# Performance work log

Measured on AMD Instinct MI355X. Metric: run time of the kernel, lower is better.

## Reference

```python
import jax, jax.numpy as jnp
import numpy as np

HID = 128  # hidden_channel
C = 256    # feat_channel

def conv1x1(x, w, b):
    # x: [N, Cin, H, W], w: [Cout, Cin], b: [Cout]
    return jnp.einsum('nchw,oc->nohw', x, w) + b[None, :, None, None]

def maxpool2(x):
    N, Ch, H, W = x.shape
    return x.reshape(N, Ch, H // 2, 2, W // 2, 2).max(axis=(3, 5))

def setup_inputs() -> dict:
    key = jax.random.key(0)
    ks = jax.random.split(key, 6)
    rois = jax.random.normal(ks[0], (128, C, 14, 14), dtype=jnp.float32)
    feature = jax.random.normal(ks[1], (2, C, 64, 64), dtype=jnp.float32)
    s_in = 1.0 / np.sqrt(C)
    s_hid = 1.0 / np.sqrt(HID)
    wq = jax.random.uniform(ks[2], (HID, C), minval=-s_in, maxval=s_in, dtype=jnp.float32)
    wk = jax.random.uniform(ks[3], (HID, C), minval=-s_in, maxval=s_in, dtype=jnp.float32)
    wv = jax.random.uniform(ks[4], (HID, C), minval=-s_in, maxval=s_in, dtype=jnp.float32)
    wre = jax.random.uniform(ks[5], (C, HID), minval=-s_hid, maxval=s_hid, dtype=jnp.float32)
    return {
        'rois': rois, 'feature': feature,
        'wq': wq, 'bq': jnp.zeros((HID,), jnp.float32),
        'wk': wk, 'bk': jnp.zeros((HID,), jnp.float32),
        'wv': wv, 'bv': jnp.zeros((HID,), jnp.float32),
        'wre': wre, 'bre': jnp.zeros((C,), jnp.float32),
    }

def reference(rois, feature, wq, bq, wk, bk, wv, bv, wre, bre):
    BS_roinum, Cf, h, w = rois.shape
    BS = feature.shape[0]
    roinum = BS_roinum // BS
    _h, _w = h // 2, w // 2

    # Q at full resolution
    q = conv1x1(rois, wq, bq)                              # [BS*R, HID, h, w]
    q = q.transpose(0, 2, 3, 1).reshape(BS, roinum * h * w, HID)

    ds = maxpool2(rois)                                    # [BS*R, C, _h, _w]
    k = conv1x1(ds, wk, bk).transpose(0, 2, 3, 1).reshape(BS, roinum * _h * _w, HID)
    v = conv1x1(ds, wv, bv).transpose(0, 2, 3, 1).reshape(BS, roinum * _h * _w, HID)

    score = jnp.einsum('bqc,bkc->bqk', q, k)               # [BS, R*h*w, R*_h*_w]
    score = jax.nn.softmax(score, axis=-1)
    y = jnp.einsum('bqk,bkc->bqc', score, v)               # [BS, R*h*w, HID]

    y = y.reshape(BS * roinum, h, w, HID).transpose(0, 3, 1, 2)
    y = conv1x1(y, wre, bre)                               # [BS*R, C, h, w]
    return rois + y
```

## Files before the change

kernel.cpp:

```cpp
#include <hip/hip_runtime.h>
#include <math.h>

constexpr int CIN  = 256;
constexpr int HID  = 128;
constexpr int P    = 196;
constexpr int PP   = 49;
constexpr int NQ   = 12544;
constexpr int NKEY = 3136;
constexpr int NS   = 5;

using f32x4 = __attribute__((ext_vector_type(4))) float;
using s16x8 = __attribute__((ext_vector_type(8))) short;
using s16x4 = __attribute__((ext_vector_type(4))) short;
using u32x2 = __attribute__((ext_vector_type(2))) unsigned int;

#define GLOBAL_AS(p) ((const void __attribute__((address_space(1)))*)(p))
#define LDS_AS(p)    ((void __attribute__((address_space(3)))*)(p))

__device__ __forceinline__ unsigned short f2bf(float x) {
    unsigned int u = __float_as_uint(x);
    u += 0x7FFFu + ((u >> 16) & 1u);
    return (unsigned short)(u >> 16);
}
__device__ __forceinline__ float bf2f(unsigned short s) {
    return __uint_as_float(((unsigned int)s) << 16);
}

__global__ __launch_bounds__(256) void prep_kernel(
    const float* __restrict__ rois,
    const float* __restrict__ wq, const float* __restrict__ wk,
    const float* __restrict__ wv, const float* __restrict__ wre,
    unsigned short* __restrict__ xq, unsigned short* __restrict__ xkv,
    unsigned short* __restrict__ wqb, unsigned short* __restrict__ wkb,
    unsigned short* __restrict__ wvb, unsigned short* __restrict__ wreb)
{
    const int bx = blockIdx.x;
    const int t  = threadIdx.x;

    if (bx >= 512) {
        const int which = bx - 512;
        const float* src = (which == 0) ? wq : (which == 1) ? wk : (which == 2) ? wv : wre;
        unsigned short* dst = (which == 0) ? wqb : (which == 1) ? wkb
                             : (which == 2) ? wvb : wreb;
        #pragma unroll 4
        for (int i = 0; i < 32; ++i) {
            const int idx = i * 256 + t;
            const float4 v = ((const float4*)src)[idx];
            s16x4 o;
            o[0] = (short)f2bf(v.x); o[1] = (short)f2bf(v.y);
            o[2] = (short)f2bf(v.z); o[3] = (short)f2bf(v.w);
            *(s16x4*)(dst + idx * 4) = o;
        }
        return;
    }

    const int n = bx >> 2;
    const int g = bx & 3;
    const int b = n >> 6, r = n & 63;
    __shared__ float xT[196 * 68];

    const int c_loc = t >> 2;
    const int pq    = t & 3;

    const float4* row4 = (const float4*)(rois + ((size_t)n * CIN + g * 64 + c_loc) * P);
    #pragma unroll
    for (int j = 0; j < 13; ++j) {
        const int idx4 = pq + 4 * j;
        if (idx4 < 49) {
            const float4 v = row4[idx4];
            xT[(idx4 * 4 + 0) * 68 + c_loc] = v.x;
            xT[(idx4 * 4 + 1) * 68 + c_loc] = v.y;
            xT[(idx4 * 4 + 2) * 68 + c_loc] = v.z;
            xT[(idx4 * 4 + 3) * 68 + c_loc] = v.w;
        }
    }
    __syncthreads();

    #pragma unroll
    for (int i = 0; i < 7; ++i) {
        const int u = i * 256 + t;
        if (u < 1568) {
            const int px = u >> 3, ch8 = (u & 7) * 8;
            s16x8 o;
            #pragma unroll
            for (int e = 0; e < 8; ++e)
                o[e] = (short)f2bf(xT[px * 68 + ch8 + e]);
            *(s16x8*)(xq + ((size_t)b * NQ + r * P + px) * CIN + g * 64 + ch8) = o;
        }
    }
    #pragma unroll
    for (int i = 0; i < 2; ++i) {
        const int u = i * 256 + t;
        if (u < 392) {
            const int pp = u >> 3, ch8 = (u & 7) * 8;
            const int py = pp / 7, px_ = pp - py * 7;
            const int base00 = (py * 2) * 14 + px_ * 2;
            s16x8 o;
            #pragma unroll
            for (int e = 0; e < 8; ++e) {
                const int c = ch8 + e;
                const float m0 = fmaxf(xT[(base00)      * 68 + c], xT[(base00 + 1)  * 68 + c]);
                const float m1 = fmaxf(xT[(base00 + 14) * 68 + c], xT[(base00 + 15) * 68 + c]);
                o[e] = (short)f2bf(fmaxf(m0, m1));
            }
            *(s16x8*)(xkv + ((size_t)b * NKEY + r * PP + pp) * CIN + g * 64 + ch8) = o;
        }
    }
}

__global__ __launch_bounds__(128) void gemm_fused_kernel(
    const unsigned short* __restrict__ xq, const unsigned short* __restrict__ xkv,
    const unsigned short* __restrict__ wqb, const unsigned short* __restrict__ wkb,
    const unsigned short* __restrict__ wvb,
    const float* __restrict__ bq, const float* __restrict__ bk, const float* __restrict__ bv,
    unsigned short* __restrict__ q, unsigned short* __restrict__ kmat,
    unsigned short* __restrict__ vt_g)
{
    const int bx = blockIdx.x;
    const unsigned short* x; const unsigned short* w; const float* bias;
    int m_blk, mode;
    if (bx < 392)      { mode = 0; x = xq;  w = wqb; bias = bq; m_blk = bx; }
    else if (bx < 490) { mode = 1; x = xkv; w = wkb; bias = bk; m_blk = bx - 392; }
    else               { mode = 2; x = xkv; w = wvb; bias = bv; m_blk = bx - 490; }

    const int t = threadIdx.x;
    const int wid = t >> 6, lane = t & 63;
    const int quad = lane >> 4, c = lane & 15;
    const int m_base = m_blk * 64;
    const int n_base = wid * 64;

    f32x4 acc[4][4];
    #pragma unroll
    for (int i = 0; i < 4; ++i)
        #pragma unroll
        for (int j = 0; j < 4; ++j) acc[i][j] = (f32x4)(0.f);

    if (mode <= 1) {
        #pragma unroll
        for (int ks = 0; ks < 8; ++ks) {
            s16x8 af[4], bf[4];
            #pragma unroll
            for (int mt = 0; mt < 4; ++mt)
                af[mt] = *(const s16x8*)(x + (size_t)(m_base + mt * 16 + c) * CIN + ks * 32 + quad * 8);
            #pragma unroll
            for (int nt = 0; nt < 4; ++nt)
                bf[nt] = *(const s16x8*)(w + (size_t)(n_base + nt * 16 + c) * CIN + ks * 32 + quad * 8);
            #pragma unroll
            for (int mt = 0; mt < 4; ++mt)
                #pragma unroll
                for (int nt = 0; nt < 4; ++nt)
                    acc[mt][nt] = __builtin_amdgcn_mfma_f32_16x16x32_bf16(bf[nt], af[mt], acc[mt][nt], 0, 0, 0);
        }
        unsigned short* out = (mode == 0) ? q : kmat;
        #pragma unroll
        for (int mt = 0; mt < 4; ++mt) {
            const int m = m_base + mt * 16 + c;
            #pragma unroll
            for (int nt = 0; nt < 4; ++nt) {
                const int n0 = n_base + nt * 16 + quad * 4;
                const float4 b4 = *(const float4*)&bias[n0];
                s16x4 o4;
                o4[0] = (short)f2bf(acc[mt][nt][0] + b4.x);
                o4[1] = (short)f2bf(acc[mt][nt][1] + b4.y);
                o4[2] = (short)f2bf(acc[mt][nt][2] + b4.z);
                o4[3] = (short)f2bf(acc[mt][nt][3] + b4.w);
                *(s16x4*)(out + (size_t)m * HID + n0) = o4;
            }
        }
    } else {
        #pragma unroll
        for (int ks = 0; ks < 8; ++ks) {
            s16x8 af[4], bf[4];
            #pragma unroll
            for (int mt = 0; mt < 4; ++mt)
                af[mt] = *(const s16x8*)(x + (size_t)(m_base + mt * 16 + c) * CIN + ks * 32 + quad * 8);
            #pragma unroll
            for (int nt = 0; nt < 4; ++nt)
                bf[nt] = *(const s16x8*)(w + (size_t)(n_base + nt * 16 + c) * CIN + ks * 32 + quad * 8);
            #pragma unroll
            for (int mt = 0; mt < 4; ++mt)
                #pragma unroll
                for (int nt = 0; nt < 4; ++nt)
                    acc[mt][nt] = __builtin_amdgcn_mfma_f32_16x16x32_bf16(af[mt], bf[nt], acc[mt][nt], 0, 0, 0);
        }
        #pragma unroll
        for (int nt = 0; nt < 4; ++nt) {
            const int d = n_base + nt * 16 + c;
            const float bv_ = bias[d];
            #pragma unroll
            for (int mt = 0; mt < 4; ++mt) {
                const int key0 = m_base + mt * 16 + quad * 4;
                const int bb = (key0 >= NKEY) ? 1 : 0;
                const int kl = key0 - bb * NKEY;
                s16x4 o4;
                #pragma unroll
                for (int rr = 0; rr < 4; ++rr)
                    o4[rr] = (short)f2bf(acc[mt][nt][rr] + bv_);
                *(s16x4*)(vt_g + ((size_t)bb * HID + d) * NKEY + kl) = o4;
            }
        }
    }
}

__global__ __launch_bounds__(256, 2) void attn_kernel(
    const unsigned short* __restrict__ q, const unsigned short* __restrict__ kmat,
    const unsigned short* __restrict__ vt_g,
    unsigned short* __restrict__ opart, float* __restrict__ lpart)
{
    const int fid  = blockIdx.x;
    const int xcd  = fid & 7, slot = fid >> 3;
    const int wg   = (xcd < 2 ? xcd * 62 : 124 + (xcd - 2) * 61) + slot;
    const int g    = wg / NS;
    const int s    = wg - g * NS;
    const int qblk = g % 49;
    const int b    = g / 49;

    const int tid  = threadIdx.x;
    const int w    = tid >> 6;
    const int lane = tid & 63;
    const int quad = lane >> 4;
    const int c    = lane & 15;
    const int qb   = qblk * 256 + w * 64;

    __shared__ unsigned short Kst[2][32 * 128];
    __shared__ unsigned short Vst[2][128 * 32];
    __shared__ unsigned short Ps[4][64 * 72];

    const unsigned short* qg = q    + (size_t)b * NQ   * HID;
    const unsigned short* kg = kmat + (size_t)b * NKEY * HID;
    const unsigned short* vt = vt_g + (size_t)b * HID  * NKEY;

    int koff[2], voff[2];
    #pragma unroll
    for (int i = 0; i < 2; ++i) {
        const int dstk = w * 2048 + (i * 64 + lane) * 16;
        koff[i] = dstk ^ (((dstk >> 8) & 7) << 4);
        const int chunk = i * 64 + lane;
        const int d = w * 32 + (chunk >> 2), sl = chunk & 3;
        voff[i] = d * (NKEY * 2) + ((sl ^ (d & 3)) * 16);
    }
    const char* kc = (const char*)kg;
    const char* vc = (const char*)vt;

    const int B6[6] = {0, 20, 40, 60, 79, 98};
    const int kt0 = B6[s], kt1 = B6[s + 1];

    {
        const char* ks_ = kc + (size_t)kt0 * 8192;
        const char* vs_ = vc + (size_t)kt0 * 64;
        #pragma unroll
        for (int i = 0; i < 2; ++i) {
            __builtin_amdgcn_global_load_lds(GLOBAL_AS(ks_ + koff[i]),
                LDS_AS((char*)&Kst[0][0] + w * 2048 + i * 1024), 16, 0, 0);
            __builtin_amdgcn_global_load_lds(GLOBAL_AS(vs_ + voff[i]),
                LDS_AS((char*)&Vst[0][0] + w * 2048 + i * 1024), 16, 0, 0);
        }
    }

    s16x8 qf[4][4];
    #pragma unroll
    for (int nt = 0; nt < 4; ++nt)
        #pragma unroll
        for (int ks = 0; ks < 4; ++ks)
            qf[nt][ks] = *(const s16x8*)(qg + (size_t)(qb + nt * 16 + c) * HID + ks * 32 + quad * 8);

    f32x4 Ob[4][8];
    #pragma unroll
    for (int nt = 0; nt < 4; ++nt)
        #pragma unroll
        for (int nd = 0; nd < 8; ++nd) Ob[nt][nd] = (f32x4)(0.f);
    float l[4] = {0.f, 0.f, 0.f, 0.f};

    __syncthreads();

    int buf = 0;
    for (int kt = kt0; kt < kt1; ++kt) {
        if (kt + 1 < kt1) {
            const char* ks_ = kc + (size_t)(kt + 1) * 8192;
            const char* vs_ = vc + (size_t)(kt + 1) * 64;
            #pragma unroll
            for (int i = 0; i < 2; ++i) {
                __builtin_amdgcn_global_load_lds(GLOBAL_AS(ks_ + koff[i]),
                    LDS_AS((char*)&Kst[buf ^ 1][0] + w * 2048 + i * 1024), 16, 0, 0);
                __builtin_amdgcn_global_load_lds(GLOBAL_AS(vs_ + voff[i]),
                    LDS_AS((char*)&Vst[buf ^ 1][0] + w * 2048 + i * 1024), 16, 0, 0);
            }
        }

        const char* Kb = (const char*)&Kst[buf][0];
        const char* Vb = (const char*)&Vst[buf][0];

        f32x4 st[2][4];
        #pragma unroll
        for (int mt = 0; mt < 2; ++mt)
            #pragma unroll
            for (int nt = 0; nt < 4; ++nt) st[mt][nt] = (f32x4)(0.f);
        #pragma unroll
        for (int mt = 0; mt < 2; ++mt) {
            const int row = mt * 16 + c;
            s16x8 kf[4];
            #pragma unroll
            for (int ks = 0; ks < 4; ++ks)
                kf[ks] = *(const s16x8*)(Kb + ((row * 256 + ks * 64 + quad * 16) ^ ((c & 7) << 4)));
            #pragma unroll
            for (int ks = 0; ks < 4; ++ks)
                #pragma unroll
                for (int nt = 0; nt < 4; ++nt)
                    st[mt][nt] = __builtin_amdgcn_mfma_f32_16x16x32_bf16(kf[ks], qf[nt][ks], st[mt][nt], 0, 0, 0);
        }

        #pragma unroll
        for (int mt = 0; mt < 2; ++mt) {
            #pragma unroll
            for (int nt = 0; nt < 4; ++nt) {
                const float e0 = __expf(st[mt][nt][0]);
                const float e1 = __expf(st[mt][nt][1]);
                const float e2 = __expf(st[mt][nt][2]);
                const float e3 = __expf(st[mt][nt][3]);
                l[nt] += (e0 + e1) + (e2 + e3);
                u32x2 pk;
                pk[0] = (unsigned int)f2bf(e0) | ((unsigned int)f2bf(e1) << 16);
                pk[1] = (unsigned int)f2bf(e2) | ((unsigned int)f2bf(e3) << 16);
                *(u32x2*)&Ps[w][(nt * 16 + c) * 72 + mt * 16 + quad * 4] = pk;
            }
        }

        s16x8 pf[4];
        #pragma unroll
        for (int nt = 0; nt < 4; ++nt)
            pf[nt] = *(const s16x8*)&Ps[w][(nt * 16 + c) * 72 + quad * 8];
        #pragma unroll
        for (int g2 = 0; g2 < 2; ++g2) {
            s16x8 vf[4];
            #pragma unroll
            for (int dd = 0; dd < 4; ++dd) {
                const int d = (g2 * 4 + dd) * 16 + c;
                vf[dd] = *(const s16x8*)(Vb + (d * 64 + ((quad ^ (d & 3)) * 16)));
            }
            #pragma unroll
            for (int dd = 0; dd < 4; ++dd)
                #pragma unroll
                for (int nt = 0; nt < 4; ++nt)
                    Ob[nt][g2 * 4 + dd] = __builtin_amdgcn_mfma_f32_16x16x32_bf16(pf[nt], vf[dd], Ob[nt][g2 * 4 + dd], 0, 0, 0);
        }

        if (kt + 1 < kt1) __syncthreads();
        buf ^= 1;
    }

    unsigned short* Op = opart + (size_t)(s * 2 + b) * NQ * HID;
    #pragma unroll
    for (int nt = 0; nt < 4; ++nt) {
        #pragma unroll
        for (int nd = 0; nd < 8; ++nd) {
            #pragma unroll
            for (int rr = 0; rr < 4; ++rr) {
                const int qrow = qb + nt * 16 + quad * 4 + rr;
                Op[(size_t)qrow * HID + nd * 16 + c] = f2bf(Ob[nt][nd][rr]);
            }
        }
    }
    #pragma unroll
    for (int nt = 0; nt < 4; ++nt) {
        l[nt] += __shfl_xor(l[nt], 16, 64);
        l[nt] += __shfl_xor(l[nt], 32, 64);
    }
    if (quad == 0) {
        float* lp = lpart + (size_t)(s * 2 + b) * NQ;
        #pragma unroll
        for (int nt = 0; nt < 4; ++nt) lp[qb + nt * 16 + c] = l[nt];
    }
}

__global__ __launch_bounds__(256) void outproj_kernel(
    const float* __restrict__ rois,
    const unsigned short* __restrict__ opart, const float* __restrict__ lpart,
    const unsigned short* __restrict__ wreb, const float* __restrict__ bre,
    float* __restrict__ out)
{
    const int t = threadIdx.x;
    const int wid = t >> 6, lane = t & 63;
    const int quad = lane >> 4, c = lane & 15;
    const int m0 = blockIdx.x * 64;
    const int b  = (m0 >= NQ) ? 1 : 0;

    __shared__ unsigned short ys[64 * 136];

    {
        const int m_loc = t >> 2, kq = t & 3;
        const int q_local = (m0 + m_loc) - b * NQ;
        float lsum = 0.f;
        #pragma unroll
        for (int sl = 0; sl < NS; ++sl)
            lsum += lpart[(size_t)(sl * 2 + b) * NQ + q_local];
        const float invl = 1.0f / lsum;
        #pragma unroll
        for (int ch = 0; ch < 4; ++ch) {
            float a8[8] = {0, 0, 0, 0, 0, 0, 0, 0};
            #pragma unroll
            for (int sl = 0; sl < NS; ++sl) {
                const s16x8 v = *(const s16x8*)&opart[
                    ((size_t)(sl * 2 + b) * NQ + q_local) * HID + kq * 32 + ch * 8];
                #pragma unroll
                for (int e = 0; e < 8; ++e) a8[e] += bf2f((unsigned short)v[e]);
            }
            s16x8 o;
            #pragma unroll
            for (int e = 0; e < 8; ++e) o[e] = (short)f2bf(a8[e] * invl);
            *(s16x8*)&ys[m_loc * 136 + kq * 32 + ch * 8] = o;
        }
    }
    __syncthreads();

    const int o_base = wid * 64;
    s16x8 wf[4][4];
    #pragma unroll
    for (int ot = 0; ot < 4; ++ot)
        #pragma unroll
        for (int ks = 0; ks < 4; ++ks)
            wf[ot][ks] = *(const s16x8*)(wreb + (size_t)(o_base + ot * 16 + c) * HID + ks * 32 + quad * 8);

    f32x4 acc[4][4];
    #pragma unroll
    for (int i = 0; i < 4; ++i)
        #pragma unroll
        for (int j = 0; j < 4; ++j) acc[i][j] = (f32x4)(0.f);

    #pragma unroll
    for (int ks = 0; ks < 4; ++ks) {
        s16x8 yf[4];
        #pragma unroll
        for (int mt = 0; mt < 4; ++mt)
            yf[mt] = *(const s16x8*)&ys[(mt * 16 + c) * 136 + ks * 32 + quad * 8];
        #pragma unroll
        for (int mt = 0; mt < 4; ++mt)
            #pragma unroll
            for (int ot = 0; ot < 4; ++ot)
                acc[mt][ot] = __builtin_amdgcn_mfma_f32_16x16x32_bf16(yf[mt], wf[ot][ks], acc[mt][ot], 0, 0, 0);
    }

    #pragma unroll
    for (int ot = 0; ot < 4; ++ot) {
        const int o = o_base + ot * 16 + c;
        const float br = bre[o];
        #pragma unroll
        for (int mt = 0; mt < 4; ++mt) {
            const int m_g = m0 + mt * 16 + quad * 4;
            const int mm  = m_g - b * NQ;
            const int r_roi = mm / 196;
            const int p     = mm - r_roi * 196;
            const int n_img = b * 64 + r_roi;
            const size_t base = ((size_t)n_img * CIN + o) * P + p;
            const float4 rv = *(const float4*)&rois[base];
            float4 ov;
            ov.x = rv.x + br + acc[mt][ot][0];
            ov.y = rv.y + br + acc[mt][ot][1];
            ov.z = rv.z + br + acc[mt][ot][2];
            ov.w = rv.w + br + acc[mt][ot][3];
            *(float4*)&out[base] = ov;
        }
    }
}

extern "C" void kernel_launch(void* const* d_in, const int* in_sizes, int n_in,
                              void* d_out, int out_size, void* d_ws, size_t ws_size,
                              hipStream_t stream)
{
    (void)in_sizes; (void)n_in; (void)out_size; (void)ws_size;
    const float* rois = (const float*)d_in[0];
    const float* wq  = (const float*)d_in[2];
    const float* bq  = (const float*)d_in[3];
    const float* wk  = (const float*)d_in[4];
    const float* bk  = (const float*)d_in[5];
    const float* wv  = (const float*)d_in[6];
    const float* bv  = (const float*)d_in[7];
    const float* wre = (const float*)d_in[8];
    const float* bre = (const float*)d_in[9];
    float* out = (float*)d_out;

    char* ws = (char*)d_ws;
    unsigned short* opart = (unsigned short*)(ws);
    unsigned short* xq    = (unsigned short*)(ws);
    unsigned short* xkv   = (unsigned short*)(ws + 12845056);
    unsigned short* wqb   = (unsigned short*)(ws + 16056320);
    unsigned short* wkb   = (unsigned short*)(ws + 16121856);
    unsigned short* wvb   = (unsigned short*)(ws + 16187392);
    unsigned short* q     = (unsigned short*)(ws + 32112640);
    unsigned short* kmat  = (unsigned short*)(ws + 38535168);
    unsigned short* vt_g  = (unsigned short*)(ws + 40140800);
    float*          lpart = (float*)         (ws + 41746432);
    unsigned short* wreb  = (unsigned short*)(ws + 42248192);

    prep_kernel<<<dim3(516), 256, 0, stream>>>(rois, wq, wk, wv, wre,
                                               xq, xkv, wqb, wkb, wvb, wreb);
    gemm_fused_kernel<<<dim3(588), 128, 0, stream>>>(xq, xkv, wqb, wkb, wvb,
                                                     bq, bk, bv, q, kmat, vt_g);
    attn_kernel<<<dim3(490), 256, 0, stream>>>(q, kmat, vt_g, opart, lpart);
    outproj_kernel<<<dim3(392), 256, 0, stream>>>(rois, opart, lpart, wreb, bre, out);
}
```

Baseline: 195.0 us.

## Fuse Q-input bf16 transpose into Q projection GEMM via swizzled LDS tile

The prep kernel no longer writes a transposed bf16 copy of the full ROI tensor (xq). Instead, the Q-projection blocks of the GEMM kernel load fp32 ROIs directly, convert and transpose them into an XOR-swizzled shared-memory tile, and feed the MFMA from LDS. This removes a roughly 12 MB write and re-read of the intermediate buffer. In exchange it adds about 33 KB of LDS per block, which may lower occupancy, and uses strided fp32 gathers across images inside each block.

```diff
diff --git a/kernel.cpp b/kernel.cpp
--- a/kernel.cpp
+++ b/kernel.cpp
@@ -30,7 +30,7 @@
     const float* __restrict__ rois,
     const float* __restrict__ wq, const float* __restrict__ wk,
     const float* __restrict__ wv, const float* __restrict__ wre,
-    unsigned short* __restrict__ xq, unsigned short* __restrict__ xkv,
+    unsigned short* __restrict__ xkv,
     unsigned short* __restrict__ wqb, unsigned short* __restrict__ wkb,
     unsigned short* __restrict__ wvb, unsigned short* __restrict__ wreb)
 {
@@ -77,18 +77,6 @@
     __syncthreads();
 
     #pragma unroll
-    for (int i = 0; i < 7; ++i) {
-        const int u = i * 256 + t;
-        if (u < 1568) {
-            const int px = u >> 3, ch8 = (u & 7) * 8;
-            s16x8 o;
-            #pragma unroll
-            for (int e = 0; e < 8; ++e)
-                o[e] = (short)f2bf(xT[px * 68 + ch8 + e]);
-            *(s16x8*)(xq + ((size_t)b * NQ + r * P + px) * CIN + g * 64 + ch8) = o;
-        }
-    }
-    #pragma unroll
     for (int i = 0; i < 2; ++i) {
         const int u = i * 256 + t;
         if (u < 392) {
@@ -109,7 +97,7 @@
 }
 
 __global__ __launch_bounds__(128) void gemm_fused_kernel(
-    const unsigned short* __restrict__ xq, const unsigned short* __restrict__ xkv,
+    const float* __restrict__ rois, const unsigned short* __restrict__ xkv,
     const unsigned short* __restrict__ wqb, const unsigned short* __restrict__ wkb,
     const unsigned short* __restrict__ wvb,
     const float* __restrict__ bq, const float* __restrict__ bk, const float* __restrict__ bv,
@@ -117,31 +105,94 @@
     unsigned short* __restrict__ vt_g)
 {
     const int bx = blockIdx.x;
-    const unsigned short* x; const unsigned short* w; const float* bias;
-    int m_blk, mode;
-    if (bx < 392)      { mode = 0; x = xq;  w = wqb; bias = bq; m_blk = bx; }
-    else if (bx < 490) { mode = 1; x = xkv; w = wkb; bias = bk; m_blk = bx - 392; }
-    else               { mode = 2; x = xkv; w = wvb; bias = bv; m_blk = bx - 490; }
-
     const int t = threadIdx.x;
     const int wid = t >> 6, lane = t & 63;
     const int quad = lane >> 4, c = lane & 15;
+
+    __shared__ unsigned short xT[64 * 264];
+
+    f32x4 acc[4][4];
+    #pragma unroll
+    for (int i = 0; i < 4; ++i)
+        #pragma unroll
+        for (int j = 0; j < 4; ++j) acc[i][j] = (f32x4)(0.f);
+
+    if (bx < 392) {
+        const int m0 = bx * 64;
+        {
+            const int c_loc = t >> 2;
+            const int pq4   = t & 3;
+            const int sw    = pq4 << 3;
+            #pragma unroll
+            for (int ci = 0; ci < 8; ++ci) {
+                const int ch = ci * 32 + c_loc;
+                #pragma unroll
+                for (int j = 0; j < 4; ++j) {
+                    const int idx4 = (m0 >> 2) + pq4 + 4 * j;
+                    const int n_img = idx4 / 49;
+                    const int p4 = idx4 - n_img * 49;
+                    const float4 v = ((const float4*)(rois + ((size_t)(n_img * CIN + ch)) * P))[p4];
+                    const int r0 = (pq4 + 4 * j) * 4;
+                    const int cs = ch ^ sw;
+                    xT[(r0 + 0) * 264 + cs] = f2bf(v.x);
+                    xT[(r0 + 1) * 264 + cs] = f2bf(v.y);
+                    xT[(r0 + 2) * 264 + cs] = f2bf(v.z);
+                    xT[(r0 + 3) * 264 + cs] = f2bf(v.w);
+                }
+            }
+        }
+        __syncthreads();
+
+        const int m_base = m0;
+        const int n_base = wid * 64;
+        const int swr = ((c >> 2) & 3) << 3;
+        #pragma unroll
+        for (int ks = 0; ks < 8; ++ks) {
+            s16x8 af[4], bf[4];
+            #pragma unroll
+            for (int mt = 0; mt < 4; ++mt)
+                af[mt] = *(const s16x8*)&xT[(mt * 16 + c) * 264 + ((ks * 32 + quad * 8) ^ swr)];
+            #pragma unroll
+            for (int nt = 0; nt < 4; ++nt)
+                bf[nt] = *(const s16x8*)(wqb + (size_t)(n_base + nt * 16 + c) * CIN + ks * 32 + quad * 8);
+            #pragma unroll
+            for (int mt = 0; mt < 4; ++mt)
+                #pragma unroll
+                for (int nt = 0; nt < 4; ++nt)
+                    acc[mt][nt] = __builtin_amdgcn_mfma_f32_16x16x32_bf16(bf[nt], af[mt], acc[mt][nt], 0, 0, 0);
+        }
+        #pragma unroll
+        for (int mt = 0; mt < 4; ++mt) {
+            const int m = m_base + mt * 16 + c;
+            #pragma unroll
+            for (int nt = 0; nt < 4; ++nt) {
+                const int n0 = n_base + nt * 16 + quad * 4;
+                const float4 b4 = *(const float4*)&bq[n0];
+                s16x4 o4;
+                o4[0] = (short)f2bf(acc[mt][nt][0] + b4.x);
+                o4[1] = (short)f2bf(acc[mt][nt][1] + b4.y);
+                o4[2] = (short)f2bf(acc[mt][nt][2] + b4.z);
+                o4[3] = (short)f2bf(acc[mt][nt][3] + b4.w);
+                *(s16x4*)(q + (size_t)m * HID + n0) = o4;
+            }
+        }
+        return;
+    }
+
+    const unsigned short* w; const float* bias;
+    int m_blk, mode;
+    if (bx < 490) { mode = 1; w = wkb; bias = bk; m_blk = bx - 392; }
+    else          { mode = 2; w = wvb; bias = bv; m_blk = bx - 490; }
     const int m_base = m_blk * 64;
     const int n_base = wid * 64;
 
-    f32x4 acc[4][4];
-    #pragma unroll
-    for (int i = 0; i < 4; ++i)
-        #pragma unroll
-        for (int j = 0; j < 4; ++j) acc[i][j] = (f32x4)(0.f);
-
-    if (mode <= 1) {
+    if (mode == 1) {
         #pragma unroll
         for (int ks = 0; ks < 8; ++ks) {
             s16x8 af[4], bf[4];
             #pragma unroll
             for (int mt = 0; mt < 4; ++mt)
-                af[mt] = *(const s16x8*)(x + (size_t)(m_base + mt * 16 + c) * CIN + ks * 32 + quad * 8);
+                af[mt] = *(const s16x8*)(xkv + (size_t)(m_base + mt * 16 + c) * CIN + ks * 32 + quad * 8);
             #pragma unroll
             for (int nt = 0; nt < 4; ++nt)
                 bf[nt] = *(const s16x8*)(w + (size_t)(n_base + nt * 16 + c) * CIN + ks * 32 + quad * 8);
@@ -151,7 +202,6 @@
                 for (int nt = 0; nt < 4; ++nt)
                     acc[mt][nt] = __builtin_amdgcn_mfma_f32_16x16x32_bf16(bf[nt], af[mt], acc[mt][nt], 0, 0, 0);
         }
-        unsigned short* out = (mode == 0) ? q : kmat;
         #pragma unroll
         for (int mt = 0; mt < 4; ++mt) {
             const int m = m_base + mt * 16 + c;
@@ -164,7 +214,7 @@
                 o4[1] = (short)f2bf(acc[mt][nt][1] + b4.y);
                 o4[2] = (short)f2bf(acc[mt][nt][2] + b4.z);
                 o4[3] = (short)f2bf(acc[mt][nt][3] + b4.w);
-                *(s16x4*)(out + (size_t)m * HID + n0) = o4;
+                *(s16x4*)(kmat + (size_t)m * HID + n0) = o4;
             }
         }
     } else {
@@ -173,7 +223,7 @@
             s16x8 af[4], bf[4];
             #pragma unroll
             for (int mt = 0; mt < 4; ++mt)
-                af[mt] = *(const s16x8*)(x + (size_t)(m_base + mt * 16 + c) * CIN + ks * 32 + quad * 8);
+                af[mt] = *(const s16x8*)(xkv + (size_t)(m_base + mt * 16 + c) * CIN + ks * 32 + quad * 8);
             #pragma unroll
             for (int nt = 0; nt < 4; ++nt)
                 bf[nt] = *(const s16x8*)(w + (size_t)(n_base + nt * 16 + c) * CIN + ks * 32 + quad * 8);
@@ -480,7 +530,6 @@
 
     char* ws = (char*)d_ws;
     unsigned short* opart = (unsigned short*)(ws);
-    unsigned short* xq    = (unsigned short*)(ws);
     unsigned short* xkv   = (unsigned short*)(ws + 12845056);
     unsigned short* wqb   = (unsigned short*)(ws + 16056320);
     unsigned short* wkb   = (unsigned short*)(ws + 16121856);
@@ -492,8 +541,8 @@
     unsigned short* wreb  = (unsigned short*)(ws + 42248192);
 
     prep_kernel<<<dim3(516), 256, 0, stream>>>(rois, wq, wk, wv, wre,
-                                               xq, xkv, wqb, wkb, wvb, wreb);
-    gemm_fused_kernel<<<dim3(588), 128, 0, stream>>>(xq, xkv, wqb, wkb, wvb,
+                                               xkv, wqb, wkb, wvb, wreb);
+    gemm_fused_kernel<<<dim3(588), 128, 0, stream>>>(rois, xkv, wqb, wkb, wvb,
                                                      bq, bk, bv, q, kmat, vt_g);
     attn_kernel<<<dim3(490), 256, 0, stream>>>(q, kmat, vt_g, opart, lpart);
     outproj_kernel<<<dim3(392), 256, 0, stream>>>(rois, opart, lpart, wreb, bre, out);
```

Result: no change. 191.2 us, median of 2 (-1.9%).
